# Performance work log

Measured on AMD Instinct MI355X. Metric: run time of the kernel, lower is better.

## Reference

```python
import jax, jax.numpy as jnp
import numpy as np
from jax import lax

B, S, D, E, K, MULT = 4, 2048, 1024, 1536, 4, 4
LN_EPS = 1e-5

def log_g(x):
    return jnp.where(x >= 0, jnp.log(jax.nn.relu(x) + 0.5), -jax.nn.softplus(-x))

def layer_norm(x, g, b):
    mu = jnp.mean(x, axis=-1, keepdims=True)
    var = jnp.mean((x - mu) ** 2, axis=-1, keepdims=True)
    return (x - mu) * lax.rsqrt(var + LN_EPS) * g + b

def setup_inputs() -> dict:
    key = jax.random.key(0)
    ks = jax.random.split(key, 16)
    s = lambda fan: 1.0 / np.sqrt(fan)
    inp = {
        'x': jax.random.normal(ks[0], (B, S, D), dtype=jnp.float32),
        'conv_dw_w': jax.random.uniform(ks[1], (D, 1, K), jnp.float32, -s(K), s(K)),
        'conv_dw_b': jax.random.uniform(ks[2], (D,), jnp.float32, -s(K), s(K)),
        'conv_pw_w': jax.random.uniform(ks[3], (D, D), jnp.float32, -s(D), s(D)),
        'conv_pw_b': jax.random.uniform(ks[4], (D,), jnp.float32, -s(D), s(D)),
        'ln1_g': jnp.ones((D,), jnp.float32),
        'ln1_b': jnp.zeros((D,), jnp.float32),
        'w_f': jax.random.uniform(ks[5], (E, D), jnp.float32, -s(D), s(D)),
        'w_i': jax.random.uniform(ks[6], (E, D), jnp.float32, -s(D), s(D)),
        'w_h': jax.random.uniform(ks[7], (E, D), jnp.float32, -s(D), s(D)),
        'w_down': jax.random.uniform(ks[8], (D, E), jnp.float32, -s(E), s(E)),
        'ln2_g': jnp.ones((D,), jnp.float32),
        'ln2_b': jnp.zeros((D,), jnp.float32),
        'mlp_w1': jax.random.uniform(ks[9], (MULT * D, D), jnp.float32, -s(D), s(D)),
        'mlp_b1': jax.random.uniform(ks[10], (MULT * D,), jnp.float32, -s(D), s(D)),
        'mlp_w2': jax.random.uniform(ks[11], (D, MULT * D), jnp.float32, -s(MULT * D), s(MULT * D)),
        'mlp_b2': jax.random.uniform(ks[12], (D,), jnp.float32, -s(MULT * D), s(MULT * D)),
    }
    return inp

def _forward(x, conv_dw_w, conv_dw_b, conv_pw_w, conv_pw_b, ln1_g, ln1_b,
             w_f, w_i, w_h, w_down, ln2_g, ln2_b, mlp_w1, mlp_b1, mlp_w2, mlp_b2):
    residual = x
    # causal depthwise conv + pointwise conv (channels-first over time)
    xc = jnp.transpose(x, (0, 2, 1))                       # (B, D, S)
    xc = jnp.pad(xc, ((0, 0), (0, 0), (K - 1, 0)))         # left causal pad
    dw = lax.conv_general_dilated(xc, conv_dw_w, (1,), 'VALID',
                                  feature_group_count=D,
                                  dimension_numbers=('NCH', 'OIH', 'NCH'))
    dw = dw + conv_dw_b[None, :, None]
    pw = jnp.einsum('bds,ed->bes', dw, conv_pw_w) + conv_pw_b[None, :, None]
    x = jnp.transpose(pw, (0, 2, 1)) + residual
    x = layer_norm(x, ln1_g, ln1_b)
    # minLSTM log-space parallel scan
    log_f = -jax.nn.softplus(-(x @ w_f.T))                 # (B, S, E)
    log_i = -jax.nn.softplus(-(x @ w_i.T))
    log_th = log_g(x @ w_h.T)
    log_h0 = jnp.full((B, 1, E), jnp.log(jnp.float32(0.5)), dtype=x.dtype)
    log_values = jnp.concatenate([log_h0, log_i + log_th], axis=1)   # (B, S+1, E)
    a_star = jnp.pad(jnp.cumsum(log_f, axis=1), ((0, 0), (1, 0), (0, 0)))
    log_h = a_star + lax.cumlogsumexp(log_values - a_star, axis=1)
    h = jnp.exp(log_h)[:, 1:]                              # (B, S, E)
    x = h @ w_down.T + residual
    x = layer_norm(x, ln2_g, ln2_b)
    # MLP (exact GELU like torch default); dropout with p=0 is identity
    hmid = jax.nn.gelu(x @ mlp_w1.T + mlp_b1, approximate=False)
    return hmid @ mlp_w2.T + mlp_b2

def reference(x, conv_dw_w, conv_dw_b, conv_pw_w, conv_pw_b, ln1_g, ln1_b,
              w_f, w_i, w_h, w_down, ln2_g, ln2_b, mlp_w1, mlp_b1, mlp_w2, mlp_b2):
    return _forward(x, conv_dw_w, conv_dw_b, conv_pw_w, conv_pw_b, ln1_g, ln1_b,
                    w_f, w_i, w_h, w_down, ln2_g, ln2_b, mlp_w1, mlp_b1, mlp_w2, mlp_b2)
```

## Files before the change

kernel.cpp:

```cpp
#include <hip/hip_runtime.h>
#include <hip/hip_bf16.h>
#include <math.h>

using bf16 = __hip_bfloat16;
typedef __attribute__((ext_vector_type(8))) short s8v;
typedef __attribute__((ext_vector_type(4))) float f32x4;

#define B_  4
#define S_  2048
#define D_  1024
#define E_  1536
#define M_  (B_*S_)
#define BE_ (B_*E_)
#define NCH 128
#define CHS (S_/NCH)
#define TS_ 16
#define DWB (M_/TS_)

__device__ __forceinline__ float b2f(bf16 h) { return __bfloat162float(h); }
__device__ __forceinline__ bf16  f2b(float f) { return __float2bfloat16(f); }
__device__ __forceinline__ float su2f(short v) {
  unsigned u = ((unsigned)(unsigned short)v) << 16;
  return __builtin_bit_cast(float, u);
}

struct __align__(8)  bh4 { bf16 h[4]; };
struct __align__(16) bh8 { bf16 h[8]; };

__device__ __forceinline__ void gld16(const void* g, void* l) {
  __builtin_amdgcn_global_load_lds((const __attribute__((address_space(1))) void*)g,
                                   (__attribute__((address_space(3))) void*)l, 16, 0, 0);
}

__global__ __launch_bounds__(256) void prep_k(const float* __restrict__ x,
                                              const float* __restrict__ cw,
                                              const float* __restrict__ cb,
                                              bf16* __restrict__ dw_out,
                                              const float* __restrict__ s0,
                                              const float* __restrict__ s1,
                                              const float* __restrict__ s2,
                                              const float* __restrict__ s3,
                                              const float* __restrict__ s4,
                                              const float* __restrict__ s5,
                                              const float* __restrict__ s6,
                                              bf16* __restrict__ wdst)
{
  if (blockIdx.x < DWB) {
    int m0 = blockIdx.x * TS_;
    int sr0 = m0 & (S_ - 1);
    int d = threadIdx.x * 4;
    float wf[4][4];
#pragma unroll
    for (int i = 0; i < 4; ++i) {
      float4 wr = *(const float4*)(cw + (d + i) * 4);
      wf[i][0] = wr.x; wf[i][1] = wr.y; wf[i][2] = wr.z; wf[i][3] = wr.w;
    }
    float4 bb = *(const float4*)(cb + d);
    float4 xr[TS_ + 3];
#pragma unroll
    for (int j = 0; j < TS_ + 3; ++j) {
      int srow = sr0 - 3 + j;
      if (srow >= 0) xr[j] = *(const float4*)(x + (size_t)(m0 - 3 + j) * D_ + d);
      else           xr[j] = make_float4(0.f, 0.f, 0.f, 0.f);
    }
#pragma unroll
    for (int t = 0; t < TS_; ++t) {
      float a0 = bb.x, a1 = bb.y, a2 = bb.z, a3 = bb.w;
#pragma unroll
      for (int k = 0; k < 4; ++k) {
        float4 xv = xr[t + k];
        a0 += xv.x * wf[0][k];
        a1 += xv.y * wf[1][k];
        a2 += xv.z * wf[2][k];
        a3 += xv.w * wf[3][k];
      }
      bh4 ov;
      ov.h[0] = f2b(a0); ov.h[1] = f2b(a1); ov.h[2] = f2b(a2); ov.h[3] = f2b(a3);
      *(bh4*)(dw_out + (size_t)(m0 + t) * D_ + d) = ov;
    }
  } else {
    size_t i = ((size_t)(blockIdx.x - DWB) * 256 + threadIdx.x) * 4;
    const float* s; size_t off;
    if (i < 4194304) {
      if (i < 1048576)      { s = s0; off = 0; }
      else if (i < 2621440) { s = s1; off = 1048576; }
      else                  { s = s2; off = 2621440; }
    } else if (i < 7340032) {
      if (i < 5767168)      { s = s3; off = 4194304; }
      else                  { s = s4; off = 5767168; }
    } else {
      if (i < 11534336)     { s = s5; off = 7340032; }
      else                  { s = s6; off = 11534336; }
    }
    float4 v = *(const float4*)(s + (i - off));
    bh4 o;
    o.h[0] = f2b(v.x); o.h[1] = f2b(v.y); o.h[2] = f2b(v.z); o.h[3] = f2b(v.w);
    *(bh4*)(wdst + i) = o;
  }
}

template<int EPI>
__device__ __forceinline__ void epi_store(float v, int row, int col, int N,
                                          const float* __restrict__ bias,
                                          const float* __restrict__ resid,
                                          bf16* outH, bf16* outH2, float* outF)
{
  size_t idx = (size_t)row * N + col;
  if constexpr (EPI == 0) {
    outH[idx] = f2b(v + bias[col] + resid[idx]);
  } else if constexpr (EPI == 1) {
    if (col < 1536) outH [(size_t)row * 1536 + col]        = f2b(v);
    else            outH2[(size_t)row * 1536 + col - 1536] = f2b(v);
  } else if constexpr (EPI == 2) {
    float gh = (v >= 0.f) ? (v + 0.5f) : (1.f / (1.f + expf(-v)));
    float iv = 1.f / (1.f + expf(-b2f(outH[idx])));
    outH[idx] = f2b(gh * iv);
  } else if constexpr (EPI == 3) {
    outH[idx] = f2b(v + resid[idx]);
  } else if constexpr (EPI == 4) {
    float u = v + bias[col];
    outH[idx] = f2b(0.5f * u * (1.f + erff(u * 0.70710678118f)));
  } else {
    outF[idx] = v + bias[col];
  }
}

template<int EPI>
__global__ __launch_bounds__(256) void gemm_ab(const bf16* __restrict__ A, int lda,
                                               const bf16* __restrict__ Bb, int ldb,
                                               const float* __restrict__ bias,
                                               const float* __restrict__ resid,
                                               bf16* outH, bf16* outH2, float* outF,
                                               int M, int N, int K)
{
  __shared__ __align__(16) bf16 lsA[128 * 64];
  __shared__ __align__(16) bf16 lsB[128 * 64];
  const int tid  = threadIdx.x;
  const int lane = tid & 63;
  const int wave = tid >> 6;
  const int gx  = gridDim.x;
  const int nwg = gx * gridDim.y;
  const int bid = blockIdx.y * gx + blockIdx.x;
  const int swz = (bid & 7) * (nwg >> 3) + (bid >> 3);
  const int m0 = (swz / gx) * 128, n0 = (swz % gx) * 128;
  const int wm = (wave >> 1) * 64, wn = (wave & 1) * 64;
  const int r = lane & 15, q = lane >> 4;
  const int sw = r & 7;
  f32x4 acc[4][4] = {};

  const bf16* pa[4]; const bf16* pb[4]; int dst[4];
#pragma unroll
  for (int i = 0; i < 4; ++i) {
    int c = i * 256 + tid;
    int row = c >> 3, cc = (c & 7) ^ (row & 7);
    pa[i] = A  + (size_t)(m0 + row) * lda + cc * 8;
    pb[i] = Bb + (size_t)(n0 + row) * ldb + cc * 8;
    dst[i] = c * 16;
  }

  for (int k0 = 0; k0 < K; k0 += 64) {
#pragma unroll
    for (int i = 0; i < 4; ++i) {
      gld16(pa[i], (char*)lsA + dst[i]);
      gld16(pb[i], (char*)lsB + dst[i]);
      pa[i] += 64; pb[i] += 64;
    }
    __syncthreads();
#pragma unroll
    for (int kk = 0; kk < 64; kk += 32) {
      const int j = (kk >> 3) + q;
      s8v af[4], bfr[4];
#pragma unroll
      for (int t = 0; t < 4; ++t) {
        af[t]  = *(const s8v*)((char*)lsA + (((wm + t * 16 + r) << 3) + (j ^ sw)) * 16);
        bfr[t] = *(const s8v*)((char*)lsB + (((wn + t * 16 + r) << 3) + (j ^ sw)) * 16);
      }
#pragma unroll
      for (int mi = 0; mi < 4; ++mi)
#pragma unroll
        for (int ni = 0; ni < 4; ++ni)
          acc[mi][ni] = __builtin_amdgcn_mfma_f32_16x16x32_bf16(af[mi], bfr[ni], acc[mi][ni], 0, 0, 0);
    }
    __syncthreads();
  }

#pragma unroll
  for (int mi = 0; mi < 4; ++mi)
#pragma unroll
    for (int j = 0; j < 4; ++j) {
      int row = m0 + wm + mi * 16 + q * 4 + j;
#pragma unroll
      for (int ni = 0; ni < 4; ++ni)
        epi_store<EPI>(acc[mi][ni][j], row, n0 + wn + ni * 16 + r, N, bias, resid, outH, outH2, outF);
    }
}

__global__ __launch_bounds__(256) void ln_k(const bf16* __restrict__ y,
                                            const float* __restrict__ g,
                                            const float* __restrict__ b,
                                            bf16* __restrict__ out)
{
  __shared__ float sm[8];
  int row = blockIdx.x;
  bh4 v4 = ((const bh4*)(y + (size_t)row * D_))[threadIdx.x];
  float v0 = b2f(v4.h[0]), v1 = b2f(v4.h[1]), v2 = b2f(v4.h[2]), v3 = b2f(v4.h[3]);
  float s = v0 + v1 + v2 + v3;
#pragma unroll
  for (int o = 32; o; o >>= 1) s += __shfl_down(s, o);
  int lane = threadIdx.x & 63, w = threadIdx.x >> 6;
  if (lane == 0) sm[w] = s;
  __syncthreads();
  float mu = (sm[0] + sm[1] + sm[2] + sm[3]) * (1.f / D_);
  float d0 = v0 - mu, d1 = v1 - mu, d2 = v2 - mu, d3 = v3 - mu;
  float qq = d0 * d0 + d1 * d1 + d2 * d2 + d3 * d3;
#pragma unroll
  for (int o = 32; o; o >>= 1) qq += __shfl_down(qq, o);
  if (lane == 0) sm[4 + w] = qq;
  __syncthreads();
  float var = (sm[4] + sm[5] + sm[6] + sm[7]) * (1.f / D_);
  float inv = rsqrtf(var + 1e-5f);
  int c = threadIdx.x * 4;
  float4 gv = *(const float4*)(g + c);
  float4 bv = *(const float4*)(b + c);
  bh4 ov;
  ov.h[0] = f2b(d0 * inv * gv.x + bv.x);
  ov.h[1] = f2b(d1 * inv * gv.y + bv.y);
  ov.h[2] = f2b(d2 * inv * gv.z + bv.z);
  ov.h[3] = f2b(d3 * inv * gv.w + bv.w);
  *(bh4*)(out + (size_t)row * D_ + c) = ov;
}

__global__ __launch_bounds__(256) void scanA2_k(const bf16* __restrict__ fpre,
                                                const bf16* __restrict__ g,
                                                float* __restrict__ Fc, float* __restrict__ Gc)
{
  int t = blockIdx.x * 256 + threadIdx.x;
  int c = t / (BE_ / 8);
  int col = t % (BE_ / 8);
  int be8 = col * 8;
  int b = be8 / E_, e = be8 % E_;
  size_t idx = (size_t)b * S_ * E_ + (size_t)c * CHS * E_ + e;
  float F[8], G[8];
#pragma unroll
  for (int j = 0; j < 8; ++j) { F[j] = 1.f; G[j] = 0.f; }
  for (int sl = 0; sl < CHS; ++sl, idx += E_) {
    s8v fv8 = *(const s8v*)(fpre + idx);
    s8v gv8 = *(const s8v*)(g + idx);
#pragma unroll
    for (int j = 0; j < 8; ++j) {
      float fv = 1.f / (1.f + expf(-su2f(fv8[j])));
      F[j] *= fv;
      G[j] = fv * G[j] + su2f(gv8[j]);
    }
  }
  size_t o = (size_t)c * BE_ + be8;
  *(float4*)(Fc + o)     = make_float4(F[0], F[1], F[2], F[3]);
  *(float4*)(Fc + o + 4) = make_float4(F[4], F[5], F[6], F[7]);
  *(float4*)(Gc + o)     = make_float4(G[0], G[1], G[2], G[3]);
  *(float4*)(Gc + o + 4) = make_float4(G[4], G[5], G[6], G[7]);
}

__global__ __launch_bounds__(256) void scanB_k(const float* __restrict__ Fc,
                                               const float* __restrict__ Gc,
                                               float* __restrict__ hst)
{
  int be = blockIdx.x * 256 + threadIdx.x;
  float h = 0.5f;
#pragma unroll 16
  for (int c = 0; c < NCH; ++c) {
    hst[c * BE_ + be] = h;
    h = Fc[c * BE_ + be] * h + Gc[c * BE_ + be];
  }
}

__global__ __launch_bounds__(256) void scanC2_k(const bf16* __restrict__ fpre,
                                                bf16* g,
                                                const float* __restrict__ hst)
{
  int t = blockIdx.x * 256 + threadIdx.x;
  int c = t / (BE_ / 8);
  int col = t % (BE_ / 8);
  int be8 = col * 8;
  int b = be8 / E_, e = be8 % E_;
  size_t idx = (size_t)b * S_ * E_ + (size_t)c * CHS * E_ + e;
  size_t o = (size_t)c * BE_ + be8;
  float4 h0 = *(const float4*)(hst + o);
  float4 h1 = *(const float4*)(hst + o + 4);
  float h[8] = {h0.x, h0.y, h0.z, h0.w, h1.x, h1.y, h1.z, h1.w};
  for (int sl = 0; sl < CHS; ++sl, idx += E_) {
    s8v fv8 = *(const s8v*)(fpre + idx);
    s8v gv8 = *(const s8v*)(g + idx);
    bh8 ov;
#pragma unroll
    for (int j = 0; j < 8; ++j) {
      float fv = 1.f / (1.f + expf(-su2f(fv8[j])));
      h[j] = fv * h[j] + su2f(gv8[j]);
      ov.h[j] = f2b(h[j]);
    }
    *(bh8*)(g + idx) = ov;
  }
}

extern "C" void kernel_launch(void* const* d_in, const int* in_sizes, int n_in,
                              void* d_out, int out_size, void* d_ws, size_t ws_size,
                              hipStream_t stream)
{
  (void)in_sizes; (void)n_in; (void)out_size; (void)ws_size;
  const float* x      = (const float*)d_in[0];
  const float* cdw_w  = (const float*)d_in[1];
  const float* cdw_b  = (const float*)d_in[2];
  const float* cpw_w  = (const float*)d_in[3];
  const float* cpw_b  = (const float*)d_in[4];
  const float* ln1_g  = (const float*)d_in[5];
  const float* ln1_b  = (const float*)d_in[6];
  const float* w_f    = (const float*)d_in[7];
  const float* w_i    = (const float*)d_in[8];
  const float* w_h    = (const float*)d_in[9];
  const float* w_down = (const float*)d_in[10];
  const float* ln2_g  = (const float*)d_in[11];
  const float* ln2_b  = (const float*)d_in[12];
  const float* mlp_w1 = (const float*)d_in[13];
  const float* mlp_b1 = (const float*)d_in[14];
  const float* mlp_w2 = (const float*)d_in[15];
  const float* mlp_b2 = (const float*)d_in[16];
  char* ws = (char*)d_ws;
  float* outF = (float*)d_out;

  bf16* dw_buf = (bf16*)(ws + 0);
  bf16* xln    = (bf16*)(ws + 0);
  float* Fc    = (float*)(ws + 0);
  float* Gc    = (float*)(ws + 3145728);
  float* hst   = (float*)(ws + 6291456);
  bf16* yb     = (bf16*)(ws + 16777216);
  bf16* hmid   = (bf16*)(ws + 16777216);
  bf16* fpre   = (bf16*)(ws + 33554432);
  bf16* gvals  = (bf16*)(ws + 58720256);
  bf16* pwb    = (bf16*)(ws + 83886080);
  bf16* wfib   = (bf16*)(ws + 85983232);
  bf16* whb    = (bf16*)(ws + 92274688);
  bf16* wdb    = (bf16*)(ws + 95420416);
  bf16* w1b    = (bf16*)(ws + 98566144);
  bf16* w2b    = (bf16*)(ws + 106954752);

  prep_k<<<DWB + 15360, 256, 0, stream>>>(x, cdw_w, cdw_b, dw_buf,
                                          cpw_w, w_f, w_i, w_h, w_down, mlp_w1, mlp_w2, pwb);

  gemm_ab<0><<<dim3(8, 64), 256, 0, stream>>>(dw_buf, D_, pwb, D_, cpw_b, x, yb, nullptr, nullptr, M_, D_, D_);
  ln_k<<<M_, 256, 0, stream>>>(yb, ln1_g, ln1_b, xln);
  gemm_ab<1><<<dim3(24, 64), 256, 0, stream>>>(xln, D_, wfib, D_, nullptr, nullptr, fpre, gvals, nullptr, M_, 3072, D_);
  gemm_ab<2><<<dim3(12, 64), 256, 0, stream>>>(xln, D_, whb, D_, nullptr, nullptr, gvals, nullptr, nullptr, M_, E_, D_);
  scanA2_k<<<(NCH*BE_/8)/256, 256, 0, stream>>>(fpre, gvals, Fc, Gc);
  scanB_k<<<BE_/256, 256, 0, stream>>>(Fc, Gc, hst);
  scanC2_k<<<(NCH*BE_/8)/256, 256, 0, stream>>>(fpre, gvals, hst);
  gemm_ab<3><<<dim3(8, 64), 256, 0, stream>>>(gvals, E_, wdb, E_, nullptr, x, yb, nullptr, nullptr, M_, D_, E_);
  ln_k<<<M_, 256, 0, stream>>>(yb, ln2_g, ln2_b, xln);
  gemm_ab<4><<<dim3(32, 64), 256, 0, stream>>>(xln, D_, w1b, D_, mlp_b1, nullptr, hmid, nullptr, nullptr, M_, 4*D_, D_);
  gemm_ab<5><<<dim3(8, 64), 256, 0, stream>>>(hmid, 4*D_, w2b, 4*D_, mlp_b2, nullptr, nullptr, nullptr, outF, M_, D_, 4*D_);
}
```

Baseline: 599.0 us.

## Switch GEMM to 32x32x16 MFMA tiles and drop block-id swizzle

```diff
diff --git a/kernel.cpp b/kernel.cpp
--- a/kernel.cpp
+++ b/kernel.cpp
@@ -4,7 +4,7 @@
 
 using bf16 = __hip_bfloat16;
 typedef __attribute__((ext_vector_type(8))) short s8v;
-typedef __attribute__((ext_vector_type(4))) float f32x4;
+typedef __attribute__((ext_vector_type(16))) float f32x16;
 
 #define B_  4
 #define S_  2048
@@ -138,15 +138,11 @@
   const int tid  = threadIdx.x;
   const int lane = tid & 63;
   const int wave = tid >> 6;
-  const int gx  = gridDim.x;
-  const int nwg = gx * gridDim.y;
-  const int bid = blockIdx.y * gx + blockIdx.x;
-  const int swz = (bid & 7) * (nwg >> 3) + (bid >> 3);
-  const int m0 = (swz / gx) * 128, n0 = (swz % gx) * 128;
+  const int m0 = blockIdx.y * 128, n0 = blockIdx.x * 128;
   const int wm = (wave >> 1) * 64, wn = (wave & 1) * 64;
-  const int r = lane & 15, q = lane >> 4;
-  const int sw = r & 7;
-  f32x4 acc[4][4] = {};
+  const int c31 = lane & 31, hi = lane >> 5;
+  const int sw31 = c31 & 7;
+  f32x16 acc[2][2] = {};
 
   const bf16* pa[4]; const bf16* pb[4]; int dst[4];
 #pragma unroll
@@ -167,32 +163,35 @@
     }
     __syncthreads();
 #pragma unroll
-    for (int kk = 0; kk < 64; kk += 32) {
-      const int j = (kk >> 3) + q;
-      s8v af[4], bfr[4];
-#pragma unroll
-      for (int t = 0; t < 4; ++t) {
-        af[t]  = *(const s8v*)((char*)lsA + (((wm + t * 16 + r) << 3) + (j ^ sw)) * 16);
-        bfr[t] = *(const s8v*)((char*)lsB + (((wn + t * 16 + r) << 3) + (j ^ sw)) * 16);
+    for (int ks = 0; ks < 4; ++ks) {
+      const int j = ks * 2 + hi;
+      s8v af[2], bf2[2];
+#pragma unroll
+      for (int t = 0; t < 2; ++t) {
+        int ra = wm + t * 32 + c31;
+        af[t]  = *(const s8v*)((char*)lsA + (((ra << 3) + (j ^ sw31)) << 4));
+        int rb = wn + t * 32 + c31;
+        bf2[t] = *(const s8v*)((char*)lsB + (((rb << 3) + (j ^ sw31)) << 4));
       }
 #pragma unroll
-      for (int mi = 0; mi < 4; ++mi)
-#pragma unroll
-        for (int ni = 0; ni < 4; ++ni)
-          acc[mi][ni] = __builtin_amdgcn_mfma_f32_16x16x32_bf16(af[mi], bfr[ni], acc[mi][ni], 0, 0, 0);
+      for (int mi = 0; mi < 2; ++mi)
+#pragma unroll
+        for (int ni = 0; ni < 2; ++ni)
+          acc[mi][ni] = __builtin_amdgcn_mfma_f32_32x32x16_bf16(af[mi], bf2[ni], acc[mi][ni], 0, 0, 0);
     }
     __syncthreads();
   }
 
 #pragma unroll
-  for (int mi = 0; mi < 4; ++mi)
-#pragma unroll
-    for (int j = 0; j < 4; ++j) {
-      int row = m0 + wm + mi * 16 + q * 4 + j;
-#pragma unroll
-      for (int ni = 0; ni < 4; ++ni)
-        epi_store<EPI>(acc[mi][ni][j], row, n0 + wn + ni * 16 + r, N, bias, resid, outH, outH2, outF);
-    }
+  for (int mi = 0; mi < 2; ++mi)
+#pragma unroll
+    for (int ni = 0; ni < 2; ++ni)
+#pragma unroll
+      for (int g = 0; g < 16; ++g) {
+        int row = m0 + wm + mi * 32 + (g & 3) + ((g >> 2) << 3) + (hi << 2);
+        int col = n0 + wn + ni * 32 + c31;
+        epi_store<EPI>(acc[mi][ni][g], row, col, N, bias, resid, outH, outH2, outF);
+      }
 }
 
 __global__ __launch_bounds__(256) void ln_k(const bf16* __restrict__ y,
```

Measured after the change: 621.9 us. 3.8% more time.

## Fuse f/i/h projections into one GEMM and move gate math into scan

Applied to the files above, without the earlier changes.

```diff
diff --git a/kernel.cpp b/kernel.cpp
--- a/kernel.cpp
+++ b/kernel.cpp
@@ -16,6 +16,8 @@
 #define CHS (S_/NCH)
 #define TS_ 16
 #define DWB (M_/TS_)
+#define FIH_I 12582912
+#define FIH_H 25165824
 
 __device__ __forceinline__ float b2f(bf16 h) { return __bfloat162float(h); }
 __device__ __forceinline__ bf16  f2b(float f) { return __float2bfloat16(f); }
@@ -23,6 +25,7 @@
   unsigned u = ((unsigned)(unsigned short)v) << 16;
   return __builtin_bit_cast(float, u);
 }
+__device__ __forceinline__ float sigm(float v) { return 1.f / (1.f + expf(-v)); }
 
 struct __align__(8)  bh4 { bf16 h[4]; };
 struct __align__(16) bh8 { bf16 h[8]; };
@@ -41,8 +44,6 @@
                                               const float* __restrict__ s2,
                                               const float* __restrict__ s3,
                                               const float* __restrict__ s4,
-                                              const float* __restrict__ s5,
-                                              const float* __restrict__ s6,
                                               bf16* __restrict__ wdst)
 {
   if (blockIdx.x < DWB) {
@@ -81,17 +82,13 @@
   } else {
     size_t i = ((size_t)(blockIdx.x - DWB) * 256 + threadIdx.x) * 4;
     const float* s; size_t off;
-    if (i < 4194304) {
+    if (i < 2621440) {
       if (i < 1048576)      { s = s0; off = 0; }
-      else if (i < 2621440) { s = s1; off = 1048576; }
-      else                  { s = s2; off = 2621440; }
-    } else if (i < 7340032) {
-      if (i < 5767168)      { s = s3; off = 4194304; }
-      else                  { s = s4; off = 5767168; }
-    } else {
-      if (i < 11534336)     { s = s5; off = 7340032; }
-      else                  { s = s6; off = 11534336; }
-    }
+      else                  { s = s1; off = 1048576; }
+    } else if (i < 5767168) {
+      if (i < 4194304)      { s = s2; off = 2621440; }
+      else                  { s = s3; off = 4194304; }
+    } else                  { s = s4; off = 5767168; }
     float4 v = *(const float4*)(s + (i - off));
     bh4 o;
     o.h[0] = f2b(v.x); o.h[1] = f2b(v.y); o.h[2] = f2b(v.z); o.h[3] = f2b(v.w);
@@ -103,24 +100,22 @@
 __device__ __forceinline__ void epi_store(float v, int row, int col, int N,
                                           const float* __restrict__ bias,
                                           const float* __restrict__ resid,
-                                          bf16* outH, bf16* outH2, float* outF)
-{
+                                          bf16* outH, float* outF)
+{
+  if constexpr (EPI == 6) {
+    int cb = col / 1536;
+    outH[(size_t)cb * FIH_I + (size_t)row * 1536 + (col - cb * 1536)] = f2b(v);
+    return;
+  }
   size_t idx = (size_t)row * N + col;
   if constexpr (EPI == 0) {
     outH[idx] = f2b(v + bias[col] + resid[idx]);
-  } else if constexpr (EPI == 1) {
-    if (col < 1536) outH [(size_t)row * 1536 + col]        = f2b(v);
-    else            outH2[(size_t)row * 1536 + col - 1536] = f2b(v);
-  } else if constexpr (EPI == 2) {
-    float gh = (v >= 0.f) ? (v + 0.5f) : (1.f / (1.f + expf(-v)));
-    float iv = 1.f / (1.f + expf(-b2f(outH[idx])));
-    outH[idx] = f2b(gh * iv);
   } else if constexpr (EPI == 3) {
     outH[idx] = f2b(v + resid[idx]);
   } else if constexpr (EPI == 4) {
     float u = v + bias[col];
     outH[idx] = f2b(0.5f * u * (1.f + erff(u * 0.70710678118f)));
-  } else {
+  } else if constexpr (EPI == 5) {
     outF[idx] = v + bias[col];
   }
 }
@@ -130,7 +125,7 @@
                                                const bf16* __restrict__ Bb, int ldb,
                                                const float* __restrict__ bias,
                                                const float* __restrict__ resid,
-                                               bf16* outH, bf16* outH2, float* outF,
+                                               bf16* outH, float* outF,
                                                int M, int N, int K)
 {
   __shared__ __align__(16) bf16 lsA[128 * 64];
@@ -138,11 +133,7 @@
   const int tid  = threadIdx.x;
   const int lane = tid & 63;
   const int wave = tid >> 6;
-  const int gx  = gridDim.x;
-  const int nwg = gx * gridDim.y;
-  const int bid = blockIdx.y * gx + blockIdx.x;
-  const int swz = (bid & 7) * (nwg >> 3) + (bid >> 3);
-  const int m0 = (swz / gx) * 128, n0 = (swz % gx) * 128;
+  const int m0 = blockIdx.y * 128, n0 = blockIdx.x * 128;
   const int wm = (wave >> 1) * 64, wn = (wave & 1) * 64;
   const int r = lane & 15, q = lane >> 4;
   const int sw = r & 7;
@@ -191,15 +182,31 @@
       int row = m0 + wm + mi * 16 + q * 4 + j;
 #pragma unroll
       for (int ni = 0; ni < 4; ++ni)
-        epi_store<EPI>(acc[mi][ni][j], row, n0 + wn + ni * 16 + r, N, bias, resid, outH, outH2, outF);
-    }
-}
-
+        epi_store<EPI>(acc[mi][ni][j], row, n0 + wn + ni * 16 + r, N, bias, resid, outH, outF);
+    }
+}
+
+template<int CVT>
 __global__ __launch_bounds__(256) void ln_k(const bf16* __restrict__ y,
                                             const float* __restrict__ g,
                                             const float* __restrict__ b,
-                                            bf16* __restrict__ out)
-{
+                                            bf16* __restrict__ out,
+                                            const float* __restrict__ cs1,
+                                            const float* __restrict__ cs2,
+                                            bf16* __restrict__ cd)
+{
+  if constexpr (CVT) {
+    if (blockIdx.x >= M_) {
+      size_t i = ((size_t)(blockIdx.x - M_) * 256 + threadIdx.x) * 4;
+      const float* s = (i < 4194304) ? cs1 : cs2;
+      size_t off = (i < 4194304) ? 0 : 4194304;
+      float4 v = *(const float4*)(s + (i - off));
+      bh4 o;
+      o.h[0] = f2b(v.x); o.h[1] = f2b(v.y); o.h[2] = f2b(v.z); o.h[3] = f2b(v.w);
+      *(bh4*)(cd + i) = o;
+      return;
+    }
+  }
   __shared__ float sm[8];
   int row = blockIdx.x;
   bh4 v4 = ((const bh4*)(y + (size_t)row * D_))[threadIdx.x];
@@ -230,8 +237,7 @@
   *(bh4*)(out + (size_t)row * D_ + c) = ov;
 }
 
-__global__ __launch_bounds__(256) void scanA2_k(const bf16* __restrict__ fpre,
-                                                const bf16* __restrict__ g,
+__global__ __launch_bounds__(256) void scanA2_k(const bf16* __restrict__ FIH,
                                                 float* __restrict__ Fc, float* __restrict__ Gc)
 {
   int t = blockIdx.x * 256 + threadIdx.x;
@@ -244,13 +250,17 @@
 #pragma unroll
   for (int j = 0; j < 8; ++j) { F[j] = 1.f; G[j] = 0.f; }
   for (int sl = 0; sl < CHS; ++sl, idx += E_) {
-    s8v fv8 = *(const s8v*)(fpre + idx);
-    s8v gv8 = *(const s8v*)(g + idx);
+    s8v f8 = *(const s8v*)(FIH + idx);
+    s8v i8 = *(const s8v*)(FIH + FIH_I + idx);
+    s8v h8 = *(const s8v*)(FIH + FIH_H + idx);
 #pragma unroll
     for (int j = 0; j < 8; ++j) {
-      float fv = 1.f / (1.f + expf(-su2f(fv8[j])));
+      float fv = sigm(su2f(f8[j]));
+      float hv = su2f(h8[j]);
+      float gh = (hv >= 0.f) ? (hv + 0.5f) : sigm(hv);
+      float gv = gh * sigm(su2f(i8[j]));
       F[j] *= fv;
-      G[j] = fv * G[j] + su2f(gv8[j]);
+      G[j] = fv * G[j] + gv;
     }
   }
   size_t o = (size_t)c * BE_ + be8;
@@ -273,8 +283,7 @@
   }
 }
 
-__global__ __launch_bounds__(256) void scanC2_k(const bf16* __restrict__ fpre,
-                                                bf16* g,
+__global__ __launch_bounds__(256) void scanC2_k(bf16* __restrict__ FIH,
                                                 const float* __restrict__ hst)
 {
   int t = blockIdx.x * 256 + threadIdx.x;
@@ -288,16 +297,20 @@
   float4 h1 = *(const float4*)(hst + o + 4);
   float h[8] = {h0.x, h0.y, h0.z, h0.w, h1.x, h1.y, h1.z, h1.w};
   for (int sl = 0; sl < CHS; ++sl, idx += E_) {
-    s8v fv8 = *(const s8v*)(fpre + idx);
-    s8v gv8 = *(const s8v*)(g + idx);
+    s8v f8 = *(const s8v*)(FIH + idx);
+    s8v i8 = *(const s8v*)(FIH + FIH_I + idx);
+    s8v h8 = *(const s8v*)(FIH + FIH_H + idx);
     bh8 ov;
 #pragma unroll
     for (int j = 0; j < 8; ++j) {
-      float fv = 1.f / (1.f + expf(-su2f(fv8[j])));
-      h[j] = fv * h[j] + su2f(gv8[j]);
+      float fv = sigm(su2f(f8[j]));
+      float hv = su2f(h8[j]);
+      float gh = (hv >= 0.f) ? (hv + 0.5f) : sigm(hv);
+      float gv = gh * sigm(su2f(i8[j]));
+      h[j] = fv * h[j] + gv;
       ov.h[j] = f2b(h[j]);
     }
-    *(bh8*)(g + idx) = ov;
+    *(bh8*)(FIH + FIH_H + idx) = ov;
   }
 }
 
@@ -332,28 +345,25 @@
   float* Gc    = (float*)(ws + 3145728);
   float* hst   = (float*)(ws + 6291456);
   bf16* yb     = (bf16*)(ws + 16777216);
+  bf16* FIH    = (bf16*)(ws + 16777216);
   bf16* hmid   = (bf16*)(ws + 16777216);
-  bf16* fpre   = (bf16*)(ws + 33554432);
-  bf16* gvals  = (bf16*)(ws + 58720256);
-  bf16* pwb    = (bf16*)(ws + 83886080);
-  bf16* wfib   = (bf16*)(ws + 85983232);
-  bf16* whb    = (bf16*)(ws + 92274688);
-  bf16* wdb    = (bf16*)(ws + 95420416);
-  bf16* w1b    = (bf16*)(ws + 98566144);
-  bf16* w2b    = (bf16*)(ws + 106954752);
-
-  prep_k<<<DWB + 15360, 256, 0, stream>>>(x, cdw_w, cdw_b, dw_buf,
-                                          cpw_w, w_f, w_i, w_h, w_down, mlp_w1, mlp_w2, pwb);
-
-  gemm_ab<0><<<dim3(8, 64), 256, 0, stream>>>(dw_buf, D_, pwb, D_, cpw_b, x, yb, nullptr, nullptr, M_, D_, D_);
-  ln_k<<<M_, 256, 0, stream>>>(yb, ln1_g, ln1_b, xln);
-  gemm_ab<1><<<dim3(24, 64), 256, 0, stream>>>(xln, D_, wfib, D_, nullptr, nullptr, fpre, gvals, nullptr, M_, 3072, D_);
-  gemm_ab<2><<<dim3(12, 64), 256, 0, stream>>>(xln, D_, whb, D_, nullptr, nullptr, gvals, nullptr, nullptr, M_, E_, D_);
-  scanA2_k<<<(NCH*BE_/8)/256, 256, 0, stream>>>(fpre, gvals, Fc, Gc);
+  bf16* pwb    = (bf16*)(ws + 92274688);
+  bf16* wfib   = (bf16*)(ws + 94371840);
+  bf16* wdb    = (bf16*)(ws + 103809024);
+  bf16* w1b    = (bf16*)(ws + 92274688);
+  bf16* w2b    = (bf16*)(ws + 100663296);
+
+  prep_k<<<DWB + 7168, 256, 0, stream>>>(x, cdw_w, cdw_b, dw_buf,
+                                         cpw_w, w_f, w_i, w_h, w_down, pwb);
+
+  gemm_ab<0><<<dim3(8, 64), 256, 0, stream>>>(dw_buf, D_, pwb, D_, cpw_b, x, yb, nullptr, M_, D_, D_);
+  ln_k<0><<<M_, 256, 0, stream>>>(yb, ln1_g, ln1_b, xln, nullptr, nullptr, nullptr);
+  gemm_ab<6><<<dim3(36, 64), 256, 0, stream>>>(xln, D_, wfib, D_, nullptr, nullptr, FIH, nullptr, M_, 4608, D_);
+  scanA2_k<<<(NCH*BE_/8)/256, 256, 0, stream>>>(FIH, Fc, Gc);
   scanB_k<<<BE_/256, 256, 0, stream>>>(Fc, Gc, hst);
-  scanC2_k<<<(NCH*BE_/8)/256, 256, 0, stream>>>(fpre, gvals, hst);
-  gemm_ab<3><<<dim3(8, 64), 256, 0, stream>>>(gvals, E_, wdb, E_, nullptr, x, yb, nullptr, nullptr, M_, D_, E_);
-  ln_k<<<M_, 256, 0, stream>>>(yb, ln2_g, ln2_b, xln);
-  gemm_ab<4><<<dim3(32, 64), 256, 0, stream>>>(xln, D_, w1b, D_, mlp_b1, nullptr, hmid, nullptr, nullptr, M_, 4*D_, D_);
-  gemm_ab<5><<<dim3(8, 64), 256, 0, stream>>>(hmid, 4*D_, w2b, 4*D_, mlp_b2, nullptr, nullptr, nullptr, outF, M_, D_, 4*D_);
-}
+  scanC2_k<<<(NCH*BE_/8)/256, 256, 0, stream>>>(FIH, hst);
+  gemm_ab<3><<<dim3(8, 64), 256, 0, stream>>>(FIH + FIH_H, E_, wdb, E_, nullptr, x, yb, nullptr, M_, D_, E_);
+  ln_k<1><<<M_ + 8192, 256, 0, stream>>>(yb, ln2_g, ln2_b, xln, mlp_w1, mlp_w2, w1b);
+  gemm_ab<4><<<dim3(32, 64), 256, 0, stream>>>(xln, D_, w1b, D_, mlp_b1, nullptr, hmid, nullptr, M_, 4*D_, D_);
+  gemm_ab<5><<<dim3(8, 64), 256, 0, stream>>>(hmid, 4*D_, w2b, 4*D_, mlp_b2, nullptr, nullptr, outF, M_, D_, 4*D_);
+}
```

Result: slower. 626.8 us (+4.6%).

## Fold chunk-carry scan into final scan pass and drop GEMM block swizzle

Applied to the files above, without the earlier changes.

```diff
diff --git a/kernel.cpp b/kernel.cpp
--- a/kernel.cpp
+++ b/kernel.cpp
@@ -138,11 +138,7 @@
   const int tid  = threadIdx.x;
   const int lane = tid & 63;
   const int wave = tid >> 6;
-  const int gx  = gridDim.x;
-  const int nwg = gx * gridDim.y;
-  const int bid = blockIdx.y * gx + blockIdx.x;
-  const int swz = (bid & 7) * (nwg >> 3) + (bid >> 3);
-  const int m0 = (swz / gx) * 128, n0 = (swz % gx) * 128;
+  const int m0 = blockIdx.y * 128, n0 = blockIdx.x * 128;
   const int wm = (wave >> 1) * 64, wn = (wave & 1) * 64;
   const int r = lane & 15, q = lane >> 4;
   const int sw = r & 7;
@@ -260,33 +256,31 @@
   *(float4*)(Gc + o + 4) = make_float4(G[4], G[5], G[6], G[7]);
 }
 
-__global__ __launch_bounds__(256) void scanB_k(const float* __restrict__ Fc,
-                                               const float* __restrict__ Gc,
-                                               float* __restrict__ hst)
-{
-  int be = blockIdx.x * 256 + threadIdx.x;
-  float h = 0.5f;
-#pragma unroll 16
-  for (int c = 0; c < NCH; ++c) {
-    hst[c * BE_ + be] = h;
-    h = Fc[c * BE_ + be] * h + Gc[c * BE_ + be];
-  }
-}
-
 __global__ __launch_bounds__(256) void scanC2_k(const bf16* __restrict__ fpre,
                                                 bf16* g,
-                                                const float* __restrict__ hst)
+                                                const float* __restrict__ Fc,
+                                                const float* __restrict__ Gc)
 {
   int t = blockIdx.x * 256 + threadIdx.x;
   int c = t / (BE_ / 8);
   int col = t % (BE_ / 8);
   int be8 = col * 8;
   int b = be8 / E_, e = be8 % E_;
+  float h[8];
+#pragma unroll
+  for (int j = 0; j < 8; ++j) h[j] = 0.5f;
+  for (int cp = 0; cp < c; ++cp) {
+    size_t o = (size_t)cp * BE_ + be8;
+    float4 F0 = *(const float4*)(Fc + o);
+    float4 F1 = *(const float4*)(Fc + o + 4);
+    float4 G0 = *(const float4*)(Gc + o);
+    float4 G1 = *(const float4*)(Gc + o + 4);
+    h[0] = F0.x * h[0] + G0.x;  h[1] = F0.y * h[1] + G0.y;
+    h[2] = F0.z * h[2] + G0.z;  h[3] = F0.w * h[3] + G0.w;
+    h[4] = F1.x * h[4] + G1.x;  h[5] = F1.y * h[5] + G1.y;
+    h[6] = F1.z * h[6] + G1.z;  h[7] = F1.w * h[7] + G1.w;
+  }
   size_t idx = (size_t)b * S_ * E_ + (size_t)c * CHS * E_ + e;
-  size_t o = (size_t)c * BE_ + be8;
-  float4 h0 = *(const float4*)(hst + o);
-  float4 h1 = *(const float4*)(hst + o + 4);
-  float h[8] = {h0.x, h0.y, h0.z, h0.w, h1.x, h1.y, h1.z, h1.w};
   for (int sl = 0; sl < CHS; ++sl, idx += E_) {
     s8v fv8 = *(const s8v*)(fpre + idx);
     s8v gv8 = *(const s8v*)(g + idx);
@@ -330,7 +324,6 @@
   bf16* xln    = (bf16*)(ws + 0);
   float* Fc    = (float*)(ws + 0);
   float* Gc    = (float*)(ws + 3145728);
-  float* hst   = (float*)(ws + 6291456);
   bf16* yb     = (bf16*)(ws + 16777216);
   bf16* hmid   = (bf16*)(ws + 16777216);
   bf16* fpre   = (bf16*)(ws + 33554432);
@@ -350,8 +343,7 @@
   gemm_ab<1><<<dim3(24, 64), 256, 0, stream>>>(xln, D_, wfib, D_, nullptr, nullptr, fpre, gvals, nullptr, M_, 3072, D_);
   gemm_ab<2><<<dim3(12, 64), 256, 0, stream>>>(xln, D_, whb, D_, nullptr, nullptr, gvals, nullptr, nullptr, M_, E_, D_);
   scanA2_k<<<(NCH*BE_/8)/256, 256, 0, stream>>>(fpre, gvals, Fc, Gc);
-  scanB_k<<<BE_/256, 256, 0, stream>>>(Fc, Gc, hst);
-  scanC2_k<<<(NCH*BE_/8)/256, 256, 0, stream>>>(fpre, gvals, hst);
+  scanC2_k<<<(NCH*BE_/8)/256, 256, 0, stream>>>(fpre, gvals, Fc, Gc);
   gemm_ab<3><<<dim3(8, 64), 256, 0, stream>>>(gvals, E_, wdb, E_, nullptr, x, yb, nullptr, nullptr, M_, D_, E_);
   ln_k<<<M_, 256, 0, stream>>>(yb, ln2_g, ln2_b, xln);
   gemm_ab<4><<<dim3(32, 64), 256, 0, stream>>>(xln, D_, w1b, D_, mlp_b1, nullptr, hmid, nullptr, nullptr, M_, 4*D_, D_);
```

After: 659.6 us. 10.1% more time.
